# Performance work log

Measured on AMD Instinct MI355X. Metric: run time of the kernel, lower is better.

The kernel has to match this reference:

```python
import jax, jax.numpy as jnp
import numpy as np

H, DH = 16, 64            # num heads, head dim
D = H * DH                # hidden size 1024
ALPHA, BW, A, R = 1.0, 1.0, 0.5, 1.0
D_INT = DH                # num_heads > 1 -> d_intrinsic = head_dim
EPS = 1e-12
CLIP = 1.0 - 1e-6         # keep acos (and its grad) finite


def setup_inputs() -> dict:
    key = jax.random.key(0)
    ks = jax.random.split(key, 5)
    w = lambda k: jax.random.normal(k, (D, D), jnp.float32) * 0.02
    return {
        "x": jax.random.normal(ks[0], (4, 1024, D), jnp.float32),
        "wq": w(ks[1]), "bq": jnp.zeros((D,), jnp.float32),
        "wk": w(ks[2]), "bk": jnp.zeros((D,), jnp.float32),
        "wv": w(ks[3]), "bv": jnp.zeros((D,), jnp.float32),
        "wo": w(ks[4]), "bo": jnp.zeros((D,), jnp.float32),
    }


def reference(x, wq, bq, wk, bk, wv, bv, wo, bo):
    B, S, _ = x.shape

    def heads(t):  # [B,S,D] -> [B,H,S,DH]
        return t.reshape(B, S, H, DH).transpose(0, 2, 1, 3)

    def l2norm(t):
        return t / jnp.maximum(jnp.linalg.norm(t, axis=-1, keepdims=True), EPS)

    q = l2norm(heads(x @ wq + bq))
    k = l2norm(heads(x @ wk + bk))
    v = heads(x @ wv + bv)

    # spherical geodesic distance
    dot = jnp.clip(jnp.einsum('bhqd,bhkd->bhqk', q, k), -CLIP, CLIP)
    g_dist = jnp.arccos(dot) * R

    # power-law kernel (alpha < 2 branch)
    attn_score = (1.0 + g_dist / jnp.sqrt(BW)) ** (-(D_INT + ALPHA))

    # bistochastic (Sinkhorn-like) normalization, a > 0 branch
    n_r = attn_score.sum(-1)   # [B,H,S] row sums
    n_c = attn_score.sum(-2)   # [B,H,S] col sums
    k_tilde = (n_r ** (-A))[..., :, None] * attn_score * (n_c ** (-A))[..., None, :]
    probs = k_tilde / jnp.maximum(k_tilde.sum(-1, keepdims=True), EPS)  # L1 row normalize

    out = jnp.einsum('bhqk,bhkd->bhqd', probs, v)
    out = out.transpose(0, 2, 1, 3).reshape(B, S, D)
    return out @ wo + bo
```

## Files before the change

### kernel.cpp

```cpp
#include <hip/hip_runtime.h>
#include <hip/hip_bf16.h>
#include <cstdint>
#include <cstddef>

#define BATCH  4
#define SEQ    1024
#define NHEAD  16
#define DHEAD  64
#define DMODEL 1024
#define NROWS  4096
#define BH     64
#define CLIPV  0.999999f
#define PEXP   65.0f

#define QOFF   133.5f
#define QK_    490.8988764f
#define QINV   0.0020370716f
#define QC     65535.5f

typedef _Float16 h16;
typedef _Float16 half8 __attribute__((ext_vector_type(8)));
typedef _Float16 half4 __attribute__((ext_vector_type(4)));
typedef __fp16   fp16x2 __attribute__((ext_vector_type(2)));
typedef float    f32x4 __attribute__((ext_vector_type(4)));
typedef unsigned uint2v __attribute__((ext_vector_type(2)));

typedef const __attribute__((address_space(1))) void gas_void;
typedef __attribute__((address_space(3))) void las_void;
#define GLOAD_LDS16(g, l) \
    __builtin_amdgcn_global_load_lds((gas_void*)(g), (las_void*)(l), 16, 0, 0)

__device__ __forceinline__ float spfns_lg(float d) {
    d = __builtin_amdgcn_fmed3f(d, -CLIPV, CLIPV);
    float a = fabsf(d);
    float s = __builtin_amdgcn_sqrtf(1.0f - a);
    float p = -0.0187293f;
    p = fmaf(p, a,  0.0742610f);
    p = fmaf(p, a, -0.2121144f);
    p = fmaf(p, a,  1.5707288f);
    float r = s * p;
    float g = (d >= 0.0f) ? r : (3.14159265358979f - r);
    return __builtin_amdgcn_logf(1.0f + g);
}

__device__ __forceinline__ unsigned pk_h2(float lo, float hi) {
    fp16x2 v = __builtin_amdgcn_cvt_pkrtz(lo, hi);
    return __builtin_bit_cast(unsigned, v);
}

__device__ __forceinline__ half8 h8_zero() {
    half8 z;
    #pragma unroll
    for (int e = 0; e < 8; ++e) z[e] = (h16)0.f;
    return z;
}

__global__ __launch_bounds__(256) void cvt_x(const float* __restrict__ x,
                                             h16* __restrict__ xh)
{
    size_t i = ((size_t)blockIdx.x * 256 + threadIdx.x) * 8;
    float4 a = *reinterpret_cast<const float4*>(&x[i]);
    float4 b = *reinterpret_cast<const float4*>(&x[i + 4]);
    half8 o;
    o[0]=(h16)a.x; o[1]=(h16)a.y; o[2]=(h16)a.z; o[3]=(h16)a.w;
    o[4]=(h16)b.x; o[5]=(h16)b.y; o[6]=(h16)b.z; o[7]=(h16)b.w;
    *reinterpret_cast<half8*>(&xh[i]) = o;
}

__global__ __launch_bounds__(256) void wtrans(const float* __restrict__ wq,
                                              const float* __restrict__ wk,
                                              const float* __restrict__ wv,
                                              const float* __restrict__ wo,
                                              h16* __restrict__ wt3,
                                              h16* __restrict__ wot)
{
    __shared__ float T[64][65];
    const int k0 = blockIdx.x * 64, d0 = blockIdx.y * 64, z = blockIdx.z;
    const float* src = (z==0)?wq:(z==1)?wk:(z==2)?wv:wo;
    h16* dst = (z==3) ? wot : (wt3 + (size_t)z * 1024 * 1024);
    const int t = threadIdx.x;

    #pragma unroll
    for (int p = 0; p < 4; ++p) {
        int k = (t >> 4) + p * 16;
        int c = (t & 15) * 4;
        float4 v = *reinterpret_cast<const float4*>(&src[(size_t)(k0 + k) * 1024 + d0 + c]);
        T[c + 0][k] = v.x; T[c + 1][k] = v.y; T[c + 2][k] = v.z; T[c + 3][k] = v.w;
    }
    __syncthreads();
    #pragma unroll
    for (int p = 0; p < 2; ++p) {
        int dl = (t >> 3) + p * 32;
        int c  = (t & 7) * 8;
        half8 o;
        #pragma unroll
        for (int e = 0; e < 8; ++e) o[e] = (h16)T[dl][c + e];
        *reinterpret_cast<half8*>(&dst[(size_t)(d0 + dl) * 1024 + k0 + c]) = o;
    }
}

__global__ __launch_bounds__(256) void gemm_f16(const h16* __restrict__ A,
                                                const h16* __restrict__ Bt,
                                                const float* __restrict__ b0,
                                                const float* __restrict__ b1,
                                                const float* __restrict__ b2,
                                                h16* __restrict__ oq,
                                                h16* __restrict__ ok,
                                                h16* __restrict__ ovt,
                                                float* __restrict__ of32,
                                                int mode)
{
    __shared__ __align__(16) h16 As[128][64];
    __shared__ __align__(16) h16 Bs[128][64];
    const int n0 = blockIdx.x * 128, d0 = blockIdx.y * 128;
    const int t = threadIdx.x, l = t & 63, w = t >> 6;
    const int wr = (w >> 1) * 64, wc = (w & 1) * 64;
    const int lr = l >> 3, lc8 = (l & 7) * 8;

    f32x4 acc[4][4];
    #pragma unroll
    for (int i = 0; i < 4; ++i)
        #pragma unroll
        for (int j = 0; j < 4; ++j) acc[i][j] = (f32x4){0.f,0.f,0.f,0.f};

    for (int k0 = 0; k0 < 1024; k0 += 64) {
        __syncthreads();
        #pragma unroll
        for (int q = 0; q < 4; ++q) {
            int r = w * 32 + q * 8;
            GLOAD_LDS16(&A[(size_t)(n0 + r + lr) * 1024 + k0 + lc8], &As[r][0]);
            GLOAD_LDS16(&Bt[(size_t)(d0 + r + lr) * 1024 + k0 + lc8], &Bs[r][0]);
        }
        __syncthreads();
        #pragma unroll
        for (int kk = 0; kk < 2; ++kk) {
            half8 a[4], b[4];
            #pragma unroll
            for (int fi = 0; fi < 4; ++fi)
                a[fi] = *reinterpret_cast<const half8*>(&As[wr + fi*16 + (l & 15)][((l >> 4) * 8) + kk * 32]);
            #pragma unroll
            for (int fj = 0; fj < 4; ++fj)
                b[fj] = *reinterpret_cast<const half8*>(&Bs[wc + fj*16 + (l & 15)][((l >> 4) * 8) + kk * 32]);
            #pragma unroll
            for (int fi = 0; fi < 4; ++fi)
                #pragma unroll
                for (int fj = 0; fj < 4; ++fj)
                    acc[fi][fj] = __builtin_amdgcn_mfma_f32_16x16x32_f16(a[fi], b[fj], acc[fi][fj], 0, 0, 0);
        }
    }

    if (mode == 0) {
        const int dbase = d0 + wc;
        const int mat = dbase >> 10, d1b = dbase & 1023, h = d1b >> 6;
        const float* bp = (mat == 0) ? b0 : (mat == 1) ? b1 : b2;
        #pragma unroll
        for (int fi = 0; fi < 4; ++fi) {
            float vals[4][4];
            #pragma unroll
            for (int fj = 0; fj < 4; ++fj) {
                float bias = bp[d1b + fj * 16 + (l & 15)];
                #pragma unroll
                for (int rr = 0; rr < 4; ++rr) vals[fj][rr] = acc[fi][fj][rr] + bias;
            }
            if (mat < 2) {
                float ss[4];
                #pragma unroll
                for (int rr = 0; rr < 4; ++rr)
                    ss[rr] = vals[0][rr]*vals[0][rr] + vals[1][rr]*vals[1][rr]
                           + vals[2][rr]*vals[2][rr] + vals[3][rr]*vals[3][rr];
                #pragma unroll
                for (int off = 1; off < 16; off <<= 1) {
                    #pragma unroll
                    for (int rr = 0; rr < 4; ++rr) ss[rr] += __shfl_xor(ss[rr], off);
                }
                #pragma unroll
                for (int rr = 0; rr < 4; ++rr) {
                    float sc = __builtin_amdgcn_rcpf(
                        fmaxf(__builtin_amdgcn_sqrtf(ss[rr]), 1e-12f));
                    #pragma unroll
                    for (int fj = 0; fj < 4; ++fj) vals[fj][rr] *= sc;
                }
            }
            const int s0n = n0 + wr + fi * 16 + ((l >> 4) << 2);
            #pragma unroll
            for (int fj = 0; fj < 4; ++fj) {
                int dh = fj * 16 + (l & 15);
                if (mat == 2) {
                    int b = s0n >> 10, s0 = s0n & 1023;
                    half4 o;
                    #pragma unroll
                    for (int rr = 0; rr < 4; ++rr) o[rr] = (h16)vals[fj][rr];
                    *reinterpret_cast<half4*>(&ovt[(((size_t)(b * NHEAD + h)) * DHEAD + dh) * SEQ + s0]) = o;
                } else {
                    h16* dst = (mat == 0) ? oq : ok;
                    #pragma unroll
                    for (int rr = 0; rr < 4; ++rr) {
                        int n = s0n + rr, b = n >> 10, s = n & 1023;
                        dst[(((size_t)(b * NHEAD + h)) * SEQ + s) * DHEAD + dh] = (h16)vals[fj][rr];
                    }
                }
            }
        }
    } else {
        #pragma unroll
        for (int fi = 0; fi < 4; ++fi) {
            #pragma unroll
            for (int fj = 0; fj < 4; ++fj) {
                int d = d0 + wc + fj * 16 + (l & 15);
                int s0n = n0 + wr + fi * 16 + ((l >> 4) << 2);
                float bias = b0[d];
                #pragma unroll
                for (int rr = 0; rr < 4; ++rr) {
                    int n = s0n + rr;
                    of32[(size_t)n * DMODEL + d] = acc[fi][fj][rr] + bias;
                }
            }
        }
    }
}

template<int CACHED>
__global__ __launch_bounds__(256) void passA(const h16* __restrict__ qh,
                                             const h16* __restrict__ kh,
                                             float* __restrict__ nc,
                                             unsigned* __restrict__ rm_u,
                                             int* __restrict__ gacc,
                                             unsigned short* __restrict__ Sw)
{
    __shared__ __align__(16) h16 Ks[32][72];
    __shared__ float red[4][32];
    const int t = threadIdx.x, l = t & 63, w = t >> 6;
    const int id  = blockIdx.y * 32 + blockIdx.x;
    const int nid = (id & 7) * 256 + (id >> 3);
    const int jt = nid & 31, bh = nid >> 5;
    const int j0 = jt * 32;

    {
        int r = t >> 3, c = (t & 7) * 8;
        *reinterpret_cast<half8*>(&Ks[r][c]) =
            *reinterpret_cast<const half8*>(&kh[(((size_t)bh * SEQ) + j0 + r) * DHEAD + c]);
    }
    __syncthreads();

    half8 kfr[2][2];
    #pragma unroll
    for (int f = 0; f < 2; ++f)
        #pragma unroll
        for (int kk = 0; kk < 2; ++kk)
            kfr[f][kk] = *reinterpret_cast<const half8*>(&Ks[f*16 + (l & 15)][((l >> 4) * 8) + kk * 32]);

    float ncacc[8];
    #pragma unroll
    for (int x = 0; x < 8; ++x) ncacc[x] = 0.f;

    unsigned short* sp[2] = {nullptr, nullptr};
    if (CACHED) {
        size_t base = ((((size_t)(bh*16 + (jt >> 1))*16)*16 + w*4 + (jt & 1)*2) << 8)
                      + (size_t)l*4;
        sp[0] = Sw + base;
        sp[1] = sp[0] + 256;
    }

    const h16* qb = qh + ((size_t)bh * SEQ + w*16 + (l & 15)) * DHEAD + ((l >> 4) * 8);
    half8 nq0 = *reinterpret_cast<const half8*>(qb);
    half8 nq1 = *reinterpret_cast<const half8*>(qb + 32);

    #pragma unroll 2
    for (int it = 0; it < 16; ++it) {
        half8 aq0 = nq0, aq1 = nq1;
        if (it < 15) {
            const h16* qn = qb + (size_t)(it + 1) * 64 * DHEAD;
            nq0 = *reinterpret_cast<const half8*>(qn);
            nq1 = *reinterpret_cast<const half8*>(qn + 32);
        }

        float mloc = 1e30f;
        #pragma unroll
        for (int f = 0; f < 2; ++f) {
            f32x4 cfr = (f32x4){0.f,0.f,0.f,0.f};
            cfr = __builtin_amdgcn_mfma_f32_16x16x32_f16(kfr[f][0], aq0, cfr, 0, 0, 0);
            cfr = __builtin_amdgcn_mfma_f32_16x16x32_f16(kfr[f][1], aq1, cfr, 0, 0, 0);
            unsigned uq[4];
            #pragma unroll
            for (int rr = 0; rr < 4; ++rr) {
                float lg = spfns_lg(cfr[rr]);
                float tt = lg * (-PEXP);
                ncacc[f*4 + rr] += __builtin_amdgcn_exp2f(tt);
                mloc = fminf(mloc, lg);
                if (CACHED) uq[rr] = (unsigned)fmaf(tt, QK_, QC);
            }
            if (CACHED) {
                uint2v pkw;
                pkw[0] = uq[0] | (uq[1] << 16);
                pkw[1] = uq[2] | (uq[3] << 16);
                __builtin_nontemporal_store(pkw, reinterpret_cast<uint2v*>(sp[f]));
            }
        }
        if (CACHED) { sp[0] += 4096; sp[1] += 4096; }
        mloc = fminf(mloc, __shfl_xor(mloc, 16));
        mloc = fminf(mloc, __shfl_xor(mloc, 32));
        if (l < 16)
            atomicMin(&rm_u[(size_t)bh * SEQ + it*64 + w*16 + l], __float_as_uint(mloc));
    }

    #pragma unroll
    for (int x = 0; x < 8; ++x) {
        #pragma unroll
        for (int off = 1; off < 16; off <<= 1)
            ncacc[x] += __shfl_xor(ncacc[x], off);
    }
    if ((l & 15) == 0) {
        #pragma unroll
        for (int x = 0; x < 8; ++x)
            red[w][(x >> 2) * 16 + (l >> 4) * 4 + (x & 3)] = ncacc[x];
    }
    __syncthreads();
    if (t < 32) {
        float v = red[0][t] + red[1][t] + red[2][t] + red[3][t];
        nc[(size_t)bh * SEQ + j0 + t] = v;
        atomicAdd(gacc, (int)rintf(__builtin_amdgcn_logf(v) * 64.0f));
    }
}

__global__ __launch_bounds__(256) void ncprep(const float* __restrict__ nc,
                                              const unsigned* __restrict__ rm_u,
                                              const int* __restrict__ gacc,
                                              float* __restrict__ lcr,
                                              float* __restrict__ lrm)
{
    int i = blockIdx.x * 256 + threadIdx.x;
    float Lm = (float)(*gacc) / (65536.0f * 64.0f);
    lcr[i] = -0.5f * (__builtin_amdgcn_logf(nc[i]) - Lm);
    lrm[i] = -PEXP * __uint_as_float(rm_u[i]);
}

__global__ __launch_bounds__(256) void vscale(h16* __restrict__ vt,
                                              const float* __restrict__ lcr,
                                              h16* __restrict__ fh)
{
    size_t gid = (size_t)blockIdx.x * 256 + threadIdx.x;
    int jb  = (int)(gid & 127) * 8;
    int bh  = (int)(gid >> 13);
    int dhq = (int)(gid >> 7) & 63;
    const float* lp = lcr + (size_t)bh * SEQ + jb;
    float f[8];
    #pragma unroll
    for (int e = 0; e < 8; ++e) f[e] = __builtin_amdgcn_exp2f(lp[e]);
    half8 v = *reinterpret_cast<half8*>(&vt[gid * 8]);
    #pragma unroll
    for (int e = 0; e < 8; ++e) v[e] = (h16)((float)v[e] * f[e]);
    *reinterpret_cast<half8*>(&vt[gid * 8]) = v;
    if (dhq == 0) {
        half8 ff;
        #pragma unroll
        for (int e = 0; e < 8; ++e) ff[e] = (h16)f[e];
        *reinterpret_cast<half8*>(&fh[(size_t)bh * SEQ + jb]) = ff;
    }
}

__global__ __launch_bounds__(256) void passB_c(const h16* __restrict__ vt,
                                               const h16* __restrict__ fh,
                                               const float* __restrict__ lrm,
                                               const unsigned short* __restrict__ Sw,
                                               h16* __restrict__ aoh)
{
    __shared__ __align__(16) h16 Vs[64][72];
    __shared__ __align__(16) h16 Ps[4][16][72];
    const int t = threadIdx.x, l = t & 63, w = t >> 6;
    const int id  = blockIdx.y * 16 + blockIdx.x;
    const int nid = (id & 7) * 128 + (id >> 3);
    const int it = nid & 15, bh = nid >> 4;
    const int i0 = it * 64;

    const float nlr = -lrm[(size_t)bh * SEQ + i0 + w*16 + (l & 15)] - QOFF;
    const bool den_lane = (l & 15) == 0;

    f32x4 pv[4];
    #pragma unroll
    for (int fd = 0; fd < 4; ++fd) pv[fd] = (f32x4){0.f,0.f,0.f,0.f};
    f32x4 pvden = (f32x4){0.f,0.f,0.f,0.f};

    const int sr = t >> 3, sc = (t & 7) * 8;
    const h16* vsrc = vt + ((size_t)bh * DHEAD + sr) * SEQ + sc;
    const h16* fsrc = fh + (size_t)bh * SEQ + (l >> 4) * 8;

    auto s_ptr = [&](int jc2, int fj) -> const uint2v* {
        size_t sidx = (((((size_t)(bh*16 + jc2)*16 + it)*4 + w)*4 + fj) << 8) + (size_t)l*4;
        return reinterpret_cast<const uint2v*>(&Sw[sidx]);
    };

    half8 vr0 = *reinterpret_cast<const half8*>(vsrc);
    half8 vr1 = *reinterpret_cast<const half8*>(vsrc + (size_t)32 * SEQ);
    uint2v sv[4];
    #pragma unroll
    for (int fj = 0; fj < 4; ++fj) sv[fj] = __builtin_nontemporal_load(s_ptr(0, fj));
    half8 fa = h8_zero(), fb = h8_zero();
    if (den_lane) {
        fa = *reinterpret_cast<const half8*>(fsrc);
        fb = *reinterpret_cast<const half8*>(fsrc + 32);
    }

    for (int jc = 0; jc < 16; ++jc) {
        __syncthreads();
        *reinterpret_cast<half8*>(&Vs[sr][sc])      = vr0;
        *reinterpret_cast<half8*>(&Vs[sr + 32][sc]) = vr1;
        __syncthreads();

        if (jc < 15) {
            const h16* vn = vsrc + (jc + 1) * 64;
            vr0 = *reinterpret_cast<const half8*>(vn);
            vr1 = *reinterpret_cast<const half8*>(vn + (size_t)32 * SEQ);
        }

        #pragma unroll
        for (int fj = 0; fj < 4; ++fj) {
            float u0 = (float)(sv[fj][0] & 0xffffu), u1 = (float)(sv[fj][0] >> 16);
            float u2 = (float)(sv[fj][1] & 0xffffu), u3 = (float)(sv[fj][1] >> 16);
            float pp0 = __builtin_amdgcn_exp2f(fmaf(u0, QINV, nlr));
            float pp1 = __builtin_amdgcn_exp2f(fmaf(u1, QINV, nlr));
            float pp2 = __builtin_amdgcn_exp2f(fmaf(u2, QINV, nlr));
            float pp3 = __builtin_amdgcn_exp2f(fmaf(u3, QINV, nlr));
            uint2v pk;
            pk[0] = pk_h2(pp0, pp1);
            pk[1] = pk_h2(pp2, pp3);
            *reinterpret_cast<uint2v*>(&Ps[w][l & 15][fj*16 + (l >> 4) * 4]) = pk;
        }

        half8 cfa = fa, cfb = fb;
        if (jc < 15) {
            #pragma unroll
            for (int fj = 0; fj < 4; ++fj)
                sv[fj] = __builtin_nontemporal_load(s_ptr(jc + 1, fj));
            if (den_lane) {
                fa = *reinterpret_cast<const half8*>(fsrc + (jc + 1) * 64);
                fb = *reinterpret_cast<const half8*>(fsrc + (jc + 1) * 64 + 32);
            }
        }

        half8 pa0 = *reinterpret_cast<const half8*>(&Ps[w][l & 15][((l >> 4) * 8)]);
        half8 pa1 = *reinterpret_cast<const half8*>(&Ps[w][l & 15][((l >> 4) * 8) + 32]);
        #pragma unroll
        for (int fd = 0; fd < 4; ++fd) {
            half8 vb0 = *reinterpret_cast<const half8*>(&Vs[fd*16 + (l & 15)][((l >> 4) * 8)]);
            half8 vb1 = *reinterpret_cast<const half8*>(&Vs[fd*16 + (l & 15)][((l >> 4) * 8) + 32]);
            pv[fd] = __builtin_amdgcn_mfma_f32_16x16x32_f16(pa0, vb0, pv[fd], 0, 0, 0);
            pv[fd] = __builtin_amdgcn_mfma_f32_16x16x32_f16(pa1, vb1, pv[fd], 0, 0, 0);
        }
        pvden = __builtin_amdgcn_mfma_f32_16x16x32_f16(pa0, cfa, pvden, 0, 0, 0);
        pvden = __builtin_amdgcn_mfma_f32_16x16x32_f16(pa1, cfb, pvden, 0, 0, 0);
    }

    const int b = bh >> 4, h = bh & 15;
    #pragma unroll
    for (int rr = 0; rr < 4; ++rr) {
        float ds = __shfl(pvden[rr], l & 48);
        float inv = __builtin_amdgcn_rcpf(ds);
        int s = i0 + w * 16 + ((l >> 4) << 2) + rr;
        #pragma unroll
        for (int fd = 0; fd < 4; ++fd) {
            aoh[((size_t)(b * SEQ + s)) * DMODEL + h * DHEAD + fd * 16 + (l & 15)] =
                (h16)(pv[fd][rr] * inv);
        }
    }
}

__global__ __launch_bounds__(256) void passB_r(const h16* __restrict__ qh,
                                               const h16* __restrict__ kh,
                                               const h16* __restrict__ vt,
                                               const float* __restrict__ lcr,
                                               const float* __restrict__ lrm,
                                               h16* __restrict__ aoh)
{
    __shared__ __align__(16) h16 Ks[64][72];
    __shared__ __align__(16) h16 Vs[64][72];
    __shared__ __align__(16) h16 Ps[4][16][72];
    __shared__ float lcr_s[64];
    __shared__ float lrm_s[64];

    const int it = blockIdx.x, bh = blockIdx.y;
    const int i0 = it * 64;
    const int t = threadIdx.x, l = t & 63, w = t >> 6;
    h16* Pflat = &Ps[0][0][0];

    #pragma unroll
    for (int p = 0; p < 2; ++p) {
        int r = (t >> 3) + p * 32, c = (t & 7) * 8;
        *reinterpret_cast<half8*>(&Pflat[r * 72 + c]) =
            *reinterpret_cast<const half8*>(&qh[(((size_t)bh * SEQ) + i0 + r) * DHEAD + c]);
    }
    if (t < 64) lrm_s[t] = lrm[(size_t)bh * SEQ + i0 + t];
    __syncthreads();

    half8 aq0 = *reinterpret_cast<const half8*>(&Pflat[(w*16 + (l & 15)) * 72 + ((l >> 4) * 8)]);
    half8 aq1 = *reinterpret_cast<const half8*>(&Pflat[(w*16 + (l & 15)) * 72 + ((l >> 4) * 8) + 32]);
    const float nlr = -lrm_s[w*16 + (l & 15)];

    half8 ones8 = h8_zero();
    if ((l & 15) == 0) {
        #pragma unroll
        for (int e = 0; e < 8; ++e) ones8[e] = (h16)1.0f;
    }

    f32x4 pv[4];
    #pragma unroll
    for (int fd = 0; fd < 4; ++fd) pv[fd] = (f32x4){0.f,0.f,0.f,0.f};
    f32x4 pvden = (f32x4){0.f,0.f,0.f,0.f};

    for (int jc = 0; jc < 16; ++jc) {
        const int j0 = jc * 64;
        __syncthreads();
        #pragma unroll
        for (int p = 0; p < 2; ++p) {
            int r = (t >> 3) + p * 32, c = (t & 7) * 8;
            *reinterpret_cast<half8*>(&Ks[r][c]) =
                *reinterpret_cast<const half8*>(&kh[(((size_t)bh * SEQ) + j0 + r) * DHEAD + c]);
            *reinterpret_cast<half8*>(&Vs[r][c]) =
                *reinterpret_cast<const half8*>(&vt[(((size_t)bh * DHEAD) + r) * SEQ + j0 + c]);
        }
        if (t < 64) lcr_s[t] = lcr[(size_t)bh * SEQ + j0 + t];
        __syncthreads();

        #pragma unroll
        for (int fj = 0; fj < 4; ++fj) {
            half8 kb0 = *reinterpret_cast<const half8*>(&Ks[fj*16 + (l & 15)][((l >> 4) * 8)]);
            half8 kb1 = *reinterpret_cast<const half8*>(&Ks[fj*16 + (l & 15)][((l >> 4) * 8) + 32]);
            f32x4 cfr = (f32x4){0.f,0.f,0.f,0.f};
            cfr = __builtin_amdgcn_mfma_f32_16x16x32_f16(kb0, aq0, cfr, 0, 0, 0);
            cfr = __builtin_amdgcn_mfma_f32_16x16x32_f16(kb1, aq1, cfr, 0, 0, 0);
            float4 lc4 = *reinterpret_cast<const float4*>(&lcr_s[fj*16 + (l >> 4) * 4]);
            float pp0 = __builtin_amdgcn_exp2f(fmaf(spfns_lg(cfr[0]), -PEXP, lc4.x + nlr));
            float pp1 = __builtin_amdgcn_exp2f(fmaf(spfns_lg(cfr[1]), -PEXP, lc4.y + nlr));
            float pp2 = __builtin_amdgcn_exp2f(fmaf(spfns_lg(cfr[2]), -PEXP, lc4.z + nlr));
            float pp3 = __builtin_amdgcn_exp2f(fmaf(spfns_lg(cfr[3]), -PEXP, lc4.w + nlr));
            uint2v pk;
            pk[0] = pk_h2(pp0, pp1);
            pk[1] = pk_h2(pp2, pp3);
            *reinterpret_cast<uint2v*>(&Ps[w][l & 15][fj*16 + (l >> 4) * 4]) = pk;
        }

        half8 pa0 = *reinterpret_cast<const half8*>(&Ps[w][l & 15][((l >> 4) * 8)]);
        half8 pa1 = *reinterpret_cast<const half8*>(&Ps[w][l & 15][((l >> 4) * 8) + 32]);
        #pragma unroll
        for (int fd = 0; fd < 4; ++fd) {
            half8 vb0 = *reinterpret_cast<const half8*>(&Vs[fd*16 + (l & 15)][((l >> 4) * 8)]);
            half8 vb1 = *reinterpret_cast<const half8*>(&Vs[fd*16 + (l & 15)][((l >> 4) * 8) + 32]);
            pv[fd] = __builtin_amdgcn_mfma_f32_16x16x32_f16(pa0, vb0, pv[fd], 0, 0, 0);
            pv[fd] = __builtin_amdgcn_mfma_f32_16x16x32_f16(pa1, vb1, pv[fd], 0, 0, 0);
        }
        pvden = __builtin_amdgcn_mfma_f32_16x16x32_f16(pa0, ones8, pvden, 0, 0, 0);
        pvden = __builtin_amdgcn_mfma_f32_16x16x32_f16(pa1, ones8, pvden, 0, 0, 0);
    }

    const int b = bh >> 4, h = bh & 15;
    #pragma unroll
    for (int rr = 0; rr < 4; ++rr) {
        float ds = __shfl(pvden[rr], l & 48);
        float inv = __builtin_amdgcn_rcpf(ds);
        int s = i0 + w * 16 + ((l >> 4) << 2) + rr;
        #pragma unroll
        for (int fd = 0; fd < 4; ++fd) {
            aoh[((size_t)(b * SEQ + s)) * DMODEL + h * DHEAD + fd * 16 + (l & 15)] =
                (h16)(pv[fd][rr] * inv);
        }
    }
}

extern "C" void kernel_launch(void* const* d_in, const int* in_sizes, int n_in,
                              void* d_out, int out_size, void* d_ws, size_t ws_size,
                              hipStream_t stream)
{
    (void)in_sizes; (void)n_in; (void)out_size;
    const float* x  = (const float*)d_in[0];
    const float* wq = (const float*)d_in[1];
    const float* bq = (const float*)d_in[2];
    const float* wk = (const float*)d_in[3];
    const float* bk = (const float*)d_in[4];
    const float* wv = (const float*)d_in[5];
    const float* bv = (const float*)d_in[6];
    const float* wo = (const float*)d_in[7];
    const float* bo = (const float*)d_in[8];
    float* out = (float*)d_out;

    h16* ws16 = (h16*)d_ws;
    const size_t NX  = (size_t)NROWS * DMODEL;
    const size_t NW3 = (size_t)3 * DMODEL * DMODEL;
    const size_t NW1 = (size_t)DMODEL * DMODEL;
    const size_t NH  = (size_t)BH * SEQ * DHEAD;
    h16* xh  = ws16;
    h16* wt3 = xh  + NX;
    h16* wot = wt3 + NW3;
    h16* qh  = wot + NW1;
    h16* kh  = qh  + NH;
    h16* vt  = kh  + NH;
    h16* aoh = vt  + NH;
    float* nc  = (float*)(aoh + NX);
    float* lcr = nc  + BH * SEQ;
    float* lrm = lcr + BH * SEQ;
    unsigned* rm_u = (unsigned*)(lrm + BH * SEQ);
    int* gacc = (int*)(rm_u + BH * SEQ);
    h16* fh = (h16*)(gacc + 1);

    size_t used = (size_t)((char*)(fh + BH * SEQ) - (char*)d_ws);
    used = (used + 255) & ~(size_t)255;
    unsigned short* Sw = (unsigned short*)((char*)d_ws + used);
    const size_t SBYTES = (size_t)BH * SEQ * SEQ * 2;
    const bool cache = (ws_size >= used + SBYTES);

    hipMemsetAsync(rm_u, 0xFF, (size_t)BH * SEQ * sizeof(unsigned), stream);
    hipMemsetAsync(gacc, 0, sizeof(int), stream);

    cvt_x<<<2048, 256, 0, stream>>>(x, xh);
    wtrans<<<dim3(16, 16, 4), 256, 0, stream>>>(wq, wk, wv, wo, wt3, wot);

    gemm_f16<<<dim3(32, 24), 256, 0, stream>>>(xh, wt3, bq, bk, bv,
                                               qh, kh, vt, nullptr, 0);

    if (cache) {
        passA<1><<<dim3(32, BH), 256, 0, stream>>>(qh, kh, nc, rm_u, gacc, Sw);
        ncprep<<<256, 256, 0, stream>>>(nc, rm_u, gacc, lcr, lrm);
        vscale<<<2048, 256, 0, stream>>>(vt, lcr, fh);
        passB_c<<<dim3(16, BH), 256, 0, stream>>>(vt, fh, lrm, Sw, aoh);
    } else {
        passA<0><<<dim3(32, BH), 256, 0, stream>>>(qh, kh, nc, rm_u, gacc, Sw);
        ncprep<<<256, 256, 0, stream>>>(nc, rm_u, gacc, lcr, lrm);
        passB_r<<<dim3(16, BH), 256, 0, stream>>>(qh, kh, vt, lcr, lrm, aoh);
    }

    gemm_f16<<<dim3(32, 8), 256, 0, stream>>>(aoh, wot, bo, nullptr, nullptr,
                                              nullptr, nullptr, nullptr, out, 1);
}
```

Measured before the change: 192.8 us.

## Fold column scaling into passB exponent, drop vscale kernel, double-buffer V tile

Removes the separate vscale kernel and instead adds the per-column log-scale term to the exponent inside passB_c, so probabilities already carry the column factor and the denominator uses a ones vector. V shared memory is double-buffered, which drops one barrier per iteration. Nontemporal load/store hints on the cached score buffer are replaced with ordinary accesses. This saves a kernel launch and a read/write pass over V, at the cost of extra per-iteration loads of lcr and different fp16 rounding of the scaled probabilities.

```diff
diff --git a/kernel.cpp b/kernel.cpp
--- a/kernel.cpp
+++ b/kernel.cpp
@@ -293,7 +293,7 @@
                 uint2v pkw;
                 pkw[0] = uq[0] | (uq[1] << 16);
                 pkw[1] = uq[2] | (uq[3] << 16);
-                __builtin_nontemporal_store(pkw, reinterpret_cast<uint2v*>(sp[f]));
+                *reinterpret_cast<uint2v*>(sp[f]) = pkw;
             }
         }
         if (CACHED) { sp[0] += 4096; sp[1] += 4096; }
@@ -334,37 +334,13 @@
     lrm[i] = -PEXP * __uint_as_float(rm_u[i]);
 }
 
-__global__ __launch_bounds__(256) void vscale(h16* __restrict__ vt,
-                                              const float* __restrict__ lcr,
-                                              h16* __restrict__ fh)
-{
-    size_t gid = (size_t)blockIdx.x * 256 + threadIdx.x;
-    int jb  = (int)(gid & 127) * 8;
-    int bh  = (int)(gid >> 13);
-    int dhq = (int)(gid >> 7) & 63;
-    const float* lp = lcr + (size_t)bh * SEQ + jb;
-    float f[8];
-    #pragma unroll
-    for (int e = 0; e < 8; ++e) f[e] = __builtin_amdgcn_exp2f(lp[e]);
-    half8 v = *reinterpret_cast<half8*>(&vt[gid * 8]);
-    #pragma unroll
-    for (int e = 0; e < 8; ++e) v[e] = (h16)((float)v[e] * f[e]);
-    *reinterpret_cast<half8*>(&vt[gid * 8]) = v;
-    if (dhq == 0) {
-        half8 ff;
-        #pragma unroll
-        for (int e = 0; e < 8; ++e) ff[e] = (h16)f[e];
-        *reinterpret_cast<half8*>(&fh[(size_t)bh * SEQ + jb]) = ff;
-    }
-}
-
 __global__ __launch_bounds__(256) void passB_c(const h16* __restrict__ vt,
-                                               const h16* __restrict__ fh,
+                                               const float* __restrict__ lcr,
                                                const float* __restrict__ lrm,
                                                const unsigned short* __restrict__ Sw,
                                                h16* __restrict__ aoh)
 {
-    __shared__ __align__(16) h16 Vs[64][72];
+    __shared__ __align__(16) h16 Vs[2][64][72];
     __shared__ __align__(16) h16 Ps[4][16][72];
     const int t = threadIdx.x, l = t & 63, w = t >> 6;
     const int id  = blockIdx.y * 16 + blockIdx.x;
@@ -373,7 +349,12 @@
     const int i0 = it * 64;
 
     const float nlr = -lrm[(size_t)bh * SEQ + i0 + w*16 + (l & 15)] - QOFF;
-    const bool den_lane = (l & 15) == 0;
+
+    half8 ones8 = h8_zero();
+    if ((l & 15) == 0) {
+        #pragma unroll
+        for (int e = 0; e < 8; ++e) ones8[e] = (h16)1.0f;
+    }
 
     f32x4 pv[4];
     #pragma unroll
@@ -382,7 +363,7 @@
 
     const int sr = t >> 3, sc = (t & 7) * 8;
     const h16* vsrc = vt + ((size_t)bh * DHEAD + sr) * SEQ + sc;
-    const h16* fsrc = fh + (size_t)bh * SEQ + (l >> 4) * 8;
+    const float* lc_base = lcr + (size_t)bh * SEQ + (l >> 4) * 4;
 
     auto s_ptr = [&](int jc2, int fj) -> const uint2v* {
         size_t sidx = (((((size_t)(bh*16 + jc2)*16 + it)*4 + w)*4 + fj) << 8) + (size_t)l*4;
@@ -392,48 +373,43 @@
     half8 vr0 = *reinterpret_cast<const half8*>(vsrc);
     half8 vr1 = *reinterpret_cast<const half8*>(vsrc + (size_t)32 * SEQ);
     uint2v sv[4];
-    #pragma unroll
-    for (int fj = 0; fj < 4; ++fj) sv[fj] = __builtin_nontemporal_load(s_ptr(0, fj));
-    half8 fa = h8_zero(), fb = h8_zero();
-    if (den_lane) {
-        fa = *reinterpret_cast<const half8*>(fsrc);
-        fb = *reinterpret_cast<const half8*>(fsrc + 32);
-    }
-
+    float4 lc[4];
+    #pragma unroll
+    for (int fj = 0; fj < 4; ++fj) {
+        sv[fj] = *s_ptr(0, fj);
+        lc[fj] = *reinterpret_cast<const float4*>(&lc_base[fj*16]);
+    }
+
+    int pb = 0;
     for (int jc = 0; jc < 16; ++jc) {
-        __syncthreads();
-        *reinterpret_cast<half8*>(&Vs[sr][sc])      = vr0;
-        *reinterpret_cast<half8*>(&Vs[sr + 32][sc]) = vr1;
-        __syncthreads();
+        *reinterpret_cast<half8*>(&Vs[pb][sr][sc])      = vr0;
+        *reinterpret_cast<half8*>(&Vs[pb][sr + 32][sc]) = vr1;
 
         if (jc < 15) {
             const h16* vn = vsrc + (jc + 1) * 64;
             vr0 = *reinterpret_cast<const half8*>(vn);
             vr1 = *reinterpret_cast<const half8*>(vn + (size_t)32 * SEQ);
         }
+        __syncthreads();
 
         #pragma unroll
         for (int fj = 0; fj < 4; ++fj) {
             float u0 = (float)(sv[fj][0] & 0xffffu), u1 = (float)(sv[fj][0] >> 16);
             float u2 = (float)(sv[fj][1] & 0xffffu), u3 = (float)(sv[fj][1] >> 16);
-            float pp0 = __builtin_amdgcn_exp2f(fmaf(u0, QINV, nlr));
-            float pp1 = __builtin_amdgcn_exp2f(fmaf(u1, QINV, nlr));
-            float pp2 = __builtin_amdgcn_exp2f(fmaf(u2, QINV, nlr));
-            float pp3 = __builtin_amdgcn_exp2f(fmaf(u3, QINV, nlr));
+            float pp0 = __builtin_amdgcn_exp2f(fmaf(u0, QINV, lc[fj].x + nlr));
+            float pp1 = __builtin_amdgcn_exp2f(fmaf(u1, QINV, lc[fj].y + nlr));
+            float pp2 = __builtin_amdgcn_exp2f(fmaf(u2, QINV, lc[fj].z + nlr));
+            float pp3 = __builtin_amdgcn_exp2f(fmaf(u3, QINV, lc[fj].w + nlr));
             uint2v pk;
             pk[0] = pk_h2(pp0, pp1);
             pk[1] = pk_h2(pp2, pp3);
             *reinterpret_cast<uint2v*>(&Ps[w][l & 15][fj*16 + (l >> 4) * 4]) = pk;
         }
-
-        half8 cfa = fa, cfb = fb;
         if (jc < 15) {
             #pragma unroll
-            for (int fj = 0; fj < 4; ++fj)
-                sv[fj] = __builtin_nontemporal_load(s_ptr(jc + 1, fj));
-            if (den_lane) {
-                fa = *reinterpret_cast<const half8*>(fsrc + (jc + 1) * 64);
-                fb = *reinterpret_cast<const half8*>(fsrc + (jc + 1) * 64 + 32);
+            for (int fj = 0; fj < 4; ++fj) {
+                sv[fj] = *s_ptr(jc + 1, fj);
+                lc[fj] = *reinterpret_cast<const float4*>(&lc_base[(jc + 1)*64 + fj*16]);
             }
         }
 
@@ -441,13 +417,14 @@
         half8 pa1 = *reinterpret_cast<const half8*>(&Ps[w][l & 15][((l >> 4) * 8) + 32]);
         #pragma unroll
         for (int fd = 0; fd < 4; ++fd) {
-            half8 vb0 = *reinterpret_cast<const half8*>(&Vs[fd*16 + (l & 15)][((l >> 4) * 8)]);
-            half8 vb1 = *reinterpret_cast<const half8*>(&Vs[fd*16 + (l & 15)][((l >> 4) * 8) + 32]);
+            half8 vb0 = *reinterpret_cast<const half8*>(&Vs[pb][fd*16 + (l & 15)][((l >> 4) * 8)]);
+            half8 vb1 = *reinterpret_cast<const half8*>(&Vs[pb][fd*16 + (l & 15)][((l >> 4) * 8) + 32]);
             pv[fd] = __builtin_amdgcn_mfma_f32_16x16x32_f16(pa0, vb0, pv[fd], 0, 0, 0);
             pv[fd] = __builtin_amdgcn_mfma_f32_16x16x32_f16(pa1, vb1, pv[fd], 0, 0, 0);
         }
-        pvden = __builtin_amdgcn_mfma_f32_16x16x32_f16(pa0, cfa, pvden, 0, 0, 0);
-        pvden = __builtin_amdgcn_mfma_f32_16x16x32_f16(pa1, cfb, pvden, 0, 0, 0);
+        pvden = __builtin_amdgcn_mfma_f32_16x16x32_f16(pa0, ones8, pvden, 0, 0, 0);
+        pvden = __builtin_amdgcn_mfma_f32_16x16x32_f16(pa1, ones8, pvden, 0, 0, 0);
+        pb ^= 1;
     }
 
     const int b = bh >> 4, h = bh & 15;
@@ -598,9 +575,8 @@
     float* lrm = lcr + BH * SEQ;
     unsigned* rm_u = (unsigned*)(lrm + BH * SEQ);
     int* gacc = (int*)(rm_u + BH * SEQ);
-    h16* fh = (h16*)(gacc + 1);
-
-    size_t used = (size_t)((char*)(fh + BH * SEQ) - (char*)d_ws);
+
+    size_t used = (size_t)((char*)(gacc + 1) - (char*)d_ws);
     used = (used + 255) & ~(size_t)255;
     unsigned short* Sw = (unsigned short*)((char*)d_ws + used);
     const size_t SBYTES = (size_t)BH * SEQ * SEQ * 2;
@@ -618,8 +594,7 @@
     if (cache) {
         passA<1><<<dim3(32, BH), 256, 0, stream>>>(qh, kh, nc, rm_u, gacc, Sw);
         ncprep<<<256, 256, 0, stream>>>(nc, rm_u, gacc, lcr, lrm);
-        vscale<<<2048, 256, 0, stream>>>(vt, lcr, fh);
-        passB_c<<<dim3(16, BH), 256, 0, stream>>>(vt, fh, lrm, Sw, aoh);
+        passB_c<<<dim3(16, BH), 256, 0, stream>>>(vt, lcr, lrm, Sw, aoh);
     } else {
         passA<0><<<dim3(32, BH), 256, 0, stream>>>(qh, kh, nc, rm_u, gacc, Sw);
         ncprep<<<256, 256, 0, stream>>>(nc, rm_u, gacc, lcr, lrm);
```

Result: faster. 181.3 us (-6.0%).
